# Kernel optimization log

Measured on AMD Instinct MI355X. Metric: run time of the kernel, lower is better.

## Reference

```python
import jax, jax.numpy as jnp
import numpy as np

D_MODEL = 1024
D_MEMORY = 64
CAPACITY = 65536
THETA = 0.01
MAX_GRAD_NORM = 1.0
GATE_HIDDEN = 32


def _gate(x, w1, b1, w2, b2):
    # 2-layer MLP: Linear -> SiLU -> Linear -> Sigmoid, squeeze last dim
    h = jax.nn.silu(x @ w1 + b1)
    return jax.nn.sigmoid(h @ w2 + b2)[..., 0]


def _assoc_loss(memory, k, v):
    # l(M; x) = mean((softmax(k M^T / sqrt(d)) M - v)^2)
    scores = jnp.einsum('bsd,cd->bsc', k, memory) / jnp.sqrt(jnp.asarray(D_MEMORY, k.dtype))
    w = jax.nn.softmax(scores, axis=-1)          # [B,S,capacity]
    retrieved = jnp.einsum('bsc,cd->bsd', w, memory)
    return jnp.mean((retrieved - v) ** 2)


def setup_inputs() -> dict:
    key = jax.random.key(0)
    ks = jax.random.split(key, 16)
    x = jax.random.normal(ks[0], (2, 1024, D_MODEL), dtype=jnp.float32)
    memory = jax.random.normal(ks[1], (CAPACITY, D_MEMORY), dtype=jnp.float32) * 0.02
    momentum_S = jax.random.normal(ks[2], (CAPACITY, D_MEMORY), dtype=jnp.float32) * 0.01
    # projections (stored as [in, out]; torch Linear applies x @ W.T + b)
    Wk = jax.random.normal(ks[3], (D_MODEL, D_MEMORY), dtype=jnp.float32) * 0.02
    bk = jnp.zeros((D_MEMORY,), dtype=jnp.float32)
    Wv = jax.random.normal(ks[4], (D_MODEL, D_MEMORY), dtype=jnp.float32) * 0.02
    bv = jnp.zeros((D_MEMORY,), dtype=jnp.float32)
    # forget gate MLP
    fg_w1 = jax.random.normal(ks[5], (D_MODEL, GATE_HIDDEN), dtype=jnp.float32) * 0.02
    fg_b1 = jnp.zeros((GATE_HIDDEN,), dtype=jnp.float32)
    fg_w2 = jax.random.normal(ks[6], (GATE_HIDDEN, 1), dtype=jnp.float32) * 0.02
    fg_b2 = jnp.zeros((1,), dtype=jnp.float32)
    # decay gate MLP
    dg_w1 = jax.random.normal(ks[7], (D_MODEL, GATE_HIDDEN), dtype=jnp.float32) * 0.02
    dg_b1 = jnp.zeros((GATE_HIDDEN,), dtype=jnp.float32)
    dg_w2 = jax.random.normal(ks[8], (GATE_HIDDEN, 1), dtype=jnp.float32) * 0.02
    dg_b2 = jnp.zeros((1,), dtype=jnp.float32)
    return {
        'x': x, 'memory': memory, 'momentum_S': momentum_S,
        'Wk': Wk, 'bk': bk, 'Wv': Wv, 'bv': bv,
        'fg_w1': fg_w1, 'fg_b1': fg_b1, 'fg_w2': fg_w2, 'fg_b2': fg_b2,
        'dg_w1': dg_w1, 'dg_b1': dg_b1, 'dg_w2': dg_w2, 'dg_b2': dg_b2,
    }


def reference(x, memory, momentum_S, Wk, bk, Wv, bv,
              fg_w1, fg_b1, fg_w2, fg_b2, dg_w1, dg_b1, dg_w2, dg_b2):
    # NeuralMemory.update(x): surprise-gradient momentum write with gated decay
    k = x @ Wk + bk   # [B,S,d_memory]
    v = x @ Wv + bv
    loss, grad_M = jax.value_and_grad(lambda M: _assoc_loss(M, k, v))(memory)
    # gradient clipping to max norm 1.0
    gn = jnp.linalg.norm(grad_M)
    grad_M = grad_M * jnp.minimum(1.0, MAX_GRAD_NORM / gn)
    # data-dependent gates on sequence-pooled input
    x_pooled = x.mean(axis=1)                                # [B, d_model]
    alpha_t = _gate(x_pooled, fg_w1, fg_b1, fg_w2, fg_b2).mean()
    eta_t = _gate(x_pooled, dg_w1, dg_b1, dg_w2, dg_b2).mean()
    # S_t = eta * S_{t-1} - theta * grad; M_t = (1 - alpha) * M_{t-1} + S_t
    S_new = eta_t * momentum_S - THETA * grad_M
    M_new = (1.0 - alpha_t) * memory + S_new
    return loss, M_new, S_new
```

## Files before the change

### kernel.cpp

```cpp
#include <hip/hip_runtime.h>
#include <math.h>

#define D_MODEL 1024
#define DMEM 64
#define CAP 65536
#define SEQ 1024
#define NTOT 2048
#define GATE_H 32
#define THETA 0.01f
#define ISQD 0.125f
#define LOG2E 1.4426950408889634f
#define LN2 0.6931471805599453f
#define NSPLIT 8
#define CSPL (CAP / NSPLIT)
#define GN_BLOCKS 2048

typedef float f32x4 __attribute__((ext_vector_type(4)));
typedef short bf16x8 __attribute__((ext_vector_type(8)));
typedef unsigned int u32x4 __attribute__((ext_vector_type(4)));
typedef unsigned int u32x2 __attribute__((ext_vector_type(2)));

#define MFMA16(a, b, c) __builtin_amdgcn_mfma_f32_16x16x32_bf16(a, b, c, 0, 0, 0)

__device__ inline unsigned short f2bf(float f) {
  union { float f; unsigned u; } v; v.f = f;
  unsigned r = v.u + 0x7FFFu + ((v.u >> 16) & 1u);
  return (unsigned short)(r >> 16);
}
__device__ inline unsigned cvtpk(float lo, float hi) {
  unsigned r;
  asm("v_cvt_pk_bf16_f32 %0, %1, %2" : "=v"(r) : "v"(lo), "v"(hi));
  return r;
}
__device__ inline float exp2i(float x) {
  float r;
  asm("v_exp_f32 %0, %1" : "=v"(r) : "v"(x));
  return r;
}

__global__ __launch_bounds__(256) void k_packm(const float* __restrict__ mem,
                                               unsigned short* __restrict__ Msb,
                                               unsigned short* __restrict__ MsbT) {
  __shared__ __align__(16) short tile[64][72];
  int tid = threadIdx.x;
  int c0 = blockIdx.x * 64;
  int r = tid >> 2, dp = (tid & 3) * 16;
  const float4* src = (const float4*)(mem + (size_t)(c0 + r) * DMEM + dp);
  float4 q0 = src[0], q1 = src[1], q2 = src[2], q3 = src[3];
  float va[16] = {q0.x, q0.y, q0.z, q0.w, q1.x, q1.y, q1.z, q1.w,
                  q2.x, q2.y, q2.z, q2.w, q3.x, q3.y, q3.z, q3.w};
  const float s1 = ISQD * LOG2E;
  union { unsigned short s[16]; u32x4 v[2]; } o;
#pragma unroll
  for (int j = 0; j < 16; ++j) o.s[j] = f2bf(va[j] * s1);
  *(u32x4*)(Msb + (size_t)(c0 + r) * DMEM + dp) = o.v[0];
  *(u32x4*)(Msb + (size_t)(c0 + r) * DMEM + dp + 8) = o.v[1];
#pragma unroll
  for (int j = 0; j < 16; ++j) tile[dp + j][r] = (short)f2bf(va[j] * ISQD);
  __syncthreads();
  int d2 = tid >> 2, cp = (tid & 3) * 16;
  u32x4 t0 = *(const u32x4*)&tile[d2][cp];
  u32x4 t1 = *(const u32x4*)&tile[d2][cp + 8];
  *(u32x4*)(MsbT + (size_t)d2 * CAP + c0 + cp) = t0;
  *(u32x4*)(MsbT + (size_t)d2 * CAP + c0 + cp + 8) = t1;
}

__global__ __launch_bounds__(256) void k_proj(const float* __restrict__ x,
    const float* __restrict__ Wk, const float* __restrict__ bk,
    const float* __restrict__ Wv, const float* __restrict__ bv,
    float* __restrict__ vout,
    unsigned short* __restrict__ kb, unsigned short* __restrict__ kbT) {
  __shared__ __align__(16) float xs[4 * D_MODEL];
  int tid = threadIdx.x;
  int r = tid >> 6, j = tid & 63;
  int nb = blockIdx.x * 4;
  const float4* xr = (const float4*)(x + (size_t)nb * D_MODEL);
  float4* xs4 = (float4*)xs;
#pragma unroll
  for (int q = 0; q < 4; ++q) xs4[tid + 256 * q] = xr[tid + 256 * q];
  __syncthreads();
  float ak = bk[j], av = bv[j];
  const float* xrow = xs + r * D_MODEL;
#pragma unroll 8
  for (int i = 0; i < D_MODEL; ++i) {
    float xv = xrow[i];
    ak = fmaf(xv, Wk[i * DMEM + j], ak);
    av = fmaf(xv, Wv[i * DMEM + j], av);
  }
  int n = nb + r;
  vout[n * DMEM + j] = av;
  kb[n * DMEM + j] = f2bf(ak);
  kbT[(size_t)j * NTOT + n] = f2bf(ak * LN2);
}

__global__ __launch_bounds__(256) void k_pool(const float* __restrict__ x,
                                              float* __restrict__ pooled) {
  int idx = blockIdx.x * 256 + threadIdx.x;
  int b = idx >> 10, j = idx & 1023;
  const float* base = x + (size_t)b * SEQ * D_MODEL + j;
  float s = 0.f;
  for (int t = 0; t < SEQ; ++t) s += base[(size_t)t * D_MODEL];
  pooled[idx] = s * (1.0f / SEQ);
}

__global__ __launch_bounds__(128) void k_gates(const float* __restrict__ pooled,
    const float* __restrict__ fw1, const float* __restrict__ fb1,
    const float* __restrict__ fw2, const float* __restrict__ fb2,
    const float* __restrict__ dw1, const float* __restrict__ db1,
    const float* __restrict__ dw2, const float* __restrict__ db2,
    float* __restrict__ scal) {
  __shared__ float hsh[2][2][GATE_H];
  __shared__ float outs[2][2];
  int t = threadIdx.x;
  int gate = t >> 6, b = (t >> 5) & 1, h = t & 31;
  const float* w1 = gate ? dw1 : fw1;
  const float* b1 = gate ? db1 : fb1;
  float z = b1[h];
  const float* prow = pooled + b * D_MODEL;
  for (int i = 0; i < D_MODEL; ++i) z = fmaf(prow[i], w1[i * GATE_H + h], z);
  float sig = 1.f / (1.f + __expf(-z));
  hsh[gate][b][h] = z * sig;
  __syncthreads();
  if (t < 4) {
    int gg = t >> 1, bb = t & 1;
    const float* w2 = gg ? dw2 : fw2;
    float zz = gg ? db2[0] : fb2[0];
    for (int hh = 0; hh < GATE_H; ++hh) zz += hsh[gg][bb][hh] * w2[hh];
    outs[gg][bb] = 1.f / (1.f + __expf(-zz));
  }
  __syncthreads();
  if (t == 0) {
    scal[0] = 0.5f * (outs[0][0] + outs[0][1]);
    scal[1] = 0.5f * (outs[1][0] + outs[1][1]);
  }
}

__global__ __launch_bounds__(256, 2) void k_fwd4(
    const unsigned short* __restrict__ kb,
    const unsigned short* __restrict__ Msb,
    const unsigned short* __restrict__ MsbT,
    float* __restrict__ l_s, float* __restrict__ r_s) {
  __shared__ __align__(16) char smem[46080];
  short* Mt  = (short*)smem;
  short* MTt = Mt + 128 * 72;
  unsigned* wtb = (unsigned*)(MTt + 64 * 136);
  int tid = threadIdx.x;
  int wv = tid >> 6, lane = tid & 63;
  int u = lane >> 4, p = lane & 15;
  int sp = blockIdx.x & 7, ng = blockIdx.x >> 3;
  int n0 = ng * 32;
  unsigned* wtp = wtb + wv * 640;

  bf16x8 bkf[2][2];
#pragma unroll
  for (int nf = 0; nf < 2; ++nf) {
    const unsigned short* kbase = kb + (size_t)(n0 + nf * 16 + p) * DMEM + u * 8;
    bkf[nf][0] = *(const bf16x8*)(kbase);
    bkf[nf][1] = *(const bf16x8*)(kbase + 32);
  }

  int mc = tid >> 3, mdh = tid & 7;
  int td = tid >> 4, tch = tid & 15;
  int c0base = sp * CSPL;
  u32x4 sM[4], sT[4];
#pragma unroll
  for (int q = 0; q < 4; ++q) {
    sM[q] = *(const u32x4*)(Msb + (size_t)(c0base + mc + 32 * q) * DMEM + mdh * 8);
    sT[q] = *(const u32x4*)(MsbT + (size_t)(td + 16 * q) * CAP + c0base + tch * 8);
  }

  f32x4 racc[4][2];
#pragma unroll
  for (int df = 0; df < 4; ++df)
#pragma unroll
    for (int nf = 0; nf < 2; ++nf) racc[df][nf] = (f32x4){0.f, 0.f, 0.f, 0.f};
  float esum0 = 0.f, esum1 = 0.f;

  const int NT = CSPL / 128;
  for (int it = 0; it < NT; ++it) {
    __syncthreads();
#pragma unroll
    for (int q = 0; q < 4; ++q) {
      *(u32x4*)(Mt + (mc + 32 * q) * 72 + mdh * 8) = sM[q];
      *(u32x4*)(MTt + (td + 16 * q) * 136 + tch * 8) = sT[q];
    }
    __syncthreads();
    int itn = (it + 1 < NT) ? it + 1 : it;
    int c0n = c0base + itn * 128;
#pragma unroll
    for (int q = 0; q < 4; ++q) {
      sM[q] = *(const u32x4*)(Msb + (size_t)(c0n + mc + 32 * q) * DMEM + mdh * 8);
      sT[q] = *(const u32x4*)(MsbT + (size_t)(td + 16 * q) * CAP + c0n + tch * 8);
    }
    f32x4 s[2][2];
#pragma unroll
    for (int cf = 0; cf < 2; ++cf) {
      bf16x8 a0 = *(const bf16x8*)(Mt + (wv * 32 + cf * 16 + p) * 72 + u * 8);
      bf16x8 a1 = *(const bf16x8*)(Mt + (wv * 32 + cf * 16 + p) * 72 + 32 + u * 8);
#pragma unroll
      for (int nf = 0; nf < 2; ++nf) {
        f32x4 acc = (f32x4){0.f, 0.f, 0.f, 0.f};
        acc = MFMA16(a0, bkf[nf][0], acc);
        acc = MFMA16(a1, bkf[nf][1], acc);
        s[cf][nf] = acc;
      }
    }
    asm volatile("" ::: "memory");
#pragma unroll
    for (int cf = 0; cf < 2; ++cf)
#pragma unroll
      for (int nf = 0; nf < 2; ++nf) {
        float e0 = exp2i(s[cf][nf].x), e1 = exp2i(s[cf][nf].y);
        float e2 = exp2i(s[cf][nf].z), e3 = exp2i(s[cf][nf].w);
        if (nf == 0) esum0 += (e0 + e1) + (e2 + e3);
        else         esum1 += (e0 + e1) + (e2 + e3);
        wtp[(nf * 16 + p) * 20 + cf * 8 + 2 * u]     = cvtpk(e0, e1);
        wtp[(nf * 16 + p) * 20 + cf * 8 + 2 * u + 1] = cvtpk(e2, e3);
      }
    asm volatile("" ::: "memory");
    u32x4 bw0 = *(const u32x4*)(wtp + p * 20 + u * 4);
    u32x4 bw1 = *(const u32x4*)(wtp + (16 + p) * 20 + u * 4);
    asm volatile("" ::: "memory");
    bf16x8 w0 = __builtin_bit_cast(bf16x8, bw0);
    bf16x8 w1 = __builtin_bit_cast(bf16x8, bw1);
#pragma unroll
    for (int df = 0; df < 4; ++df) {
      bf16x8 aT = *(const bf16x8*)(MTt + (df * 16 + p) * 136 + wv * 32 + u * 8);
      racc[df][0] = MFMA16(aT, w0, racc[df][0]);
      racc[df][1] = MFMA16(aT, w1, racc[df][1]);
    }
  }

  esum0 += __shfl_xor(esum0, 16, 64);
  esum0 += __shfl_xor(esum0, 32, 64);
  esum1 += __shfl_xor(esum1, 16, 64);
  esum1 += __shfl_xor(esum1, 32, 64);
  if (u == 0) {
    l_s[(sp * 4 + wv) * NTOT + n0 + p] = esum0;
    l_s[(sp * 4 + wv) * NTOT + n0 + 16 + p] = esum1;
  }

  __syncthreads();
  float* rt = (float*)smem;
#pragma unroll
  for (int df = 0; df < 4; ++df)
#pragma unroll
    for (int nf = 0; nf < 2; ++nf)
#pragma unroll
      for (int r = 0; r < 4; ++r)
        rt[(wv * 64 + df * 16 + 4 * u + r) * 33 + nf * 16 + p] = racc[df][nf][r];
  __syncthreads();
  int n = tid >> 3;
  int d8 = (tid & 7) * 8;
  float o[8];
#pragma unroll
  for (int q = 0; q < 8; ++q)
    o[q] = (rt[(0 * 64 + d8 + q) * 33 + n] + rt[(1 * 64 + d8 + q) * 33 + n]) +
           (rt[(2 * 64 + d8 + q) * 33 + n] + rt[(3 * 64 + d8 + q) * 33 + n]);
  float* dst = r_s + ((size_t)sp * NTOT + n0 + n) * DMEM + d8;
  *(float4*)(dst) = (float4){o[0], o[1], o[2], o[3]};
  *(float4*)(dst + 4) = (float4){o[4], o[5], o[6], o[7]};
}

__global__ __launch_bounds__(256) void k_comb(
    const float* __restrict__ l_s, const float* __restrict__ r_s,
    const float* __restrict__ v,
    unsigned short* __restrict__ gb, unsigned short* __restrict__ gbT,
    float* __restrict__ gdr8, float* __restrict__ linv,
    float* __restrict__ lossp) {
  __shared__ float lsum[4];
  int tid = threadIdx.x;
  int nl = tid >> 6, dd = tid & 63;
  int n = blockIdx.x * 4 + nl;
  float l = 0.f;
#pragma unroll
  for (int s = 0; s < 32; ++s) l += l_s[s * NTOT + n];
  float r = 0.f;
#pragma unroll
  for (int s = 0; s < NSPLIT; ++s)
    r += r_s[((size_t)s * NTOT + n) * DMEM + dd];
  float li = 1.f / l;
  float ret = r * li * 8.0f;
  float vv = v[n * DMEM + dd];
  const float c0 = 2.f / (float)(NTOT * DMEM);
  float diff = ret - vv;
  float gv = c0 * diff;
  gb[n * DMEM + dd] = f2bf(gv);
  gbT[dd * NTOT + n] = f2bf(gv);
  float gr = gv * ret;
  float lp = diff * diff;
#pragma unroll
  for (int off = 1; off < 64; off <<= 1) {
    gr += __shfl_xor(gr, off, 64);
    lp += __shfl_xor(lp, off, 64);
  }
  if (dd == 0) {
    gdr8[n] = gr * (ISQD * LOG2E);
    linv[n] = li;
    lsum[nl] = lp;
  }
  __syncthreads();
  if (tid == 0)
    lossp[blockIdx.x] =
        (lsum[0] + lsum[1] + lsum[2] + lsum[3]) * (1.f / (float)(NTOT * DMEM));
}

__global__ __launch_bounds__(256, 2) void k_bwd7(
    const unsigned short* __restrict__ kb, const unsigned short* __restrict__ kbT,
    const unsigned short* __restrict__ gb, const unsigned short* __restrict__ gbT,
    const unsigned short* __restrict__ Msb,
    const float* __restrict__ linv, const float* __restrict__ gdr8,
    float* __restrict__ gradf, unsigned short* __restrict__ gradh) {
  __shared__ __align__(16) short kt[32][72];
  __shared__ __align__(16) short gt[32][72];
  __shared__ __align__(16) short tT[2][64][40];
  __shared__ unsigned wct[4][2][1280];
  int tid = threadIdx.x;
  int wv = tid >> 6, lane = tid & 63;
  int u = lane >> 4, p = lane & 15;
  int half = blockIdx.x & 1;
  int cw = (blockIdx.x >> 1) * 256 + wv * 64;
  int nbase = half * (NTOT / 2);
  unsigned* wtp = wct[wv][0];
  unsigned* ctp = wct[wv][1];

  bf16x8 bM[4][2];
#pragma unroll
  for (int cf = 0; cf < 4; ++cf) {
    const unsigned short* mb = Msb + (size_t)(cw + cf * 16 + p) * DMEM + u * 8;
    bM[cf][0] = *(const bf16x8*)(mb);
    bM[cf][1] = *(const bf16x8*)(mb + 32);
  }

  f32x4 gacc[4][4];
#pragma unroll
  for (int cf = 0; cf < 4; ++cf)
#pragma unroll
    for (int df = 0; df < 4; ++df) gacc[cf][df] = (f32x4){0.f, 0.f, 0.f, 0.f};

  int sn = tid >> 3, sdh = tid & 7;
  int sd = tid >> 2, sch = tid & 3;

  u32x4 rk  = *(const u32x4*)(kb + (size_t)(nbase + sn) * DMEM + sdh * 8);
  u32x4 rg  = *(const u32x4*)(gb + (size_t)(nbase + sn) * DMEM + sdh * 8);
  u32x4 rkT = *(const u32x4*)(kbT + (size_t)sd * NTOT + nbase + sch * 8);
  u32x4 rgT = *(const u32x4*)(gbT + (size_t)sd * NTOT + nbase + sch * 8);

  const int NT = (NTOT / 2) / 32;
  for (int it = 0; it < NT; ++it) {
    int n0 = nbase + it * 32;
    __syncthreads();
    *(u32x4*)&kt[sn][sdh * 8] = rk;
    *(u32x4*)&gt[sn][sdh * 8] = rg;
    *(u32x4*)&tT[0][sd][sch * 8] = rkT;
    *(u32x4*)&tT[1][sd][sch * 8] = rgT;
    __syncthreads();
    {
      int n0n = (it + 1 < NT) ? n0 + 32 : n0;
      rk  = *(const u32x4*)(kb + (size_t)(n0n + sn) * DMEM + sdh * 8);
      rg  = *(const u32x4*)(gb + (size_t)(n0n + sn) * DMEM + sdh * 8);
      rkT = *(const u32x4*)(kbT + (size_t)sd * NTOT + n0n + sch * 8);
      rgT = *(const u32x4*)(gbT + (size_t)sd * NTOT + n0n + sch * 8);
    }
    asm volatile("" ::: "memory");
#pragma unroll
    for (int nf = 0; nf < 2; ++nf) {
      bf16x8 ka0 = *(const bf16x8*)&kt[nf * 16 + p][u * 8];
      bf16x8 ka1 = *(const bf16x8*)&kt[nf * 16 + p][u * 8 + 32];
      bf16x8 ga0 = *(const bf16x8*)&gt[nf * 16 + p][u * 8];
      bf16x8 ga1 = *(const bf16x8*)&gt[nf * 16 + p][u * 8 + 32];
      float4 lv = *(const float4*)(linv + n0 + nf * 16 + u * 4);
      float4 dv = *(const float4*)(gdr8 + n0 + nf * 16 + u * 4);
#pragma unroll
      for (int cf = 0; cf < 4; ++cf) {
        f32x4 s = (f32x4){0.f, 0.f, 0.f, 0.f};
        s = MFMA16(ka0, bM[cf][0], s);
        s = MFMA16(ka1, bM[cf][1], s);
        f32x4 pg = (f32x4){0.f, 0.f, 0.f, 0.f};
        pg = MFMA16(ga0, bM[cf][0], pg);
        pg = MFMA16(ga1, bM[cf][1], pg);
        float w0 = exp2i(s.x) * lv.x;
        float w1 = exp2i(s.y) * lv.y;
        float w2 = exp2i(s.z) * lv.z;
        float w3 = exp2i(s.w) * lv.w;
        float c0v = w0 * (pg.x - dv.x);
        float c1v = w1 * (pg.y - dv.y);
        float c2v = w2 * (pg.z - dv.z);
        float c3v = w3 * (pg.w - dv.w);
        wtp[(cf * 16 + p) * 20 + nf * 8 + 2 * u]     = cvtpk(w0, w1);
        wtp[(cf * 16 + p) * 20 + nf * 8 + 2 * u + 1] = cvtpk(w2, w3);
        ctp[(cf * 16 + p) * 20 + nf * 8 + 2 * u]     = cvtpk(c0v, c1v);
        ctp[(cf * 16 + p) * 20 + nf * 8 + 2 * u + 1] = cvtpk(c2v, c3v);
      }
    }
    asm volatile("" ::: "memory");
    u32x4 aw4[4], ac4[4];
#pragma unroll
    for (int cf = 0; cf < 4; ++cf) {
      aw4[cf] = *(const u32x4*)(wtp + (cf * 16 + p) * 20 + u * 4);
      ac4[cf] = *(const u32x4*)(ctp + (cf * 16 + p) * 20 + u * 4);
    }
    asm volatile("" ::: "memory");
#pragma unroll
    for (int df = 0; df < 4; ++df) {
      bf16x8 bg = *(const bf16x8*)&tT[1][df * 16 + p][u * 8];
      bf16x8 bk2 = *(const bf16x8*)&tT[0][df * 16 + p][u * 8];
#pragma unroll
      for (int cf = 0; cf < 4; ++cf) {
        gacc[cf][df] = MFMA16(__builtin_bit_cast(bf16x8, aw4[cf]), bg, gacc[cf][df]);
        gacc[cf][df] = MFMA16(__builtin_bit_cast(bf16x8, ac4[cf]), bk2, gacc[cf][df]);
      }
    }
  }

  if (half == 0) {
#pragma unroll
    for (int cf = 0; cf < 4; ++cf)
#pragma unroll
      for (int df = 0; df < 4; ++df)
#pragma unroll
        for (int r = 0; r < 4; ++r)
          gradf[(size_t)(cw + cf * 16 + 4 * u + r) * DMEM + df * 16 + p] =
              gacc[cf][df][r];
  } else {
#pragma unroll
    for (int cf = 0; cf < 4; ++cf)
#pragma unroll
      for (int df = 0; df < 4; ++df)
#pragma unroll
        for (int r = 0; r < 4; ++r)
          gradh[(size_t)(cw + cf * 16 + 4 * u + r) * DMEM + df * 16 + p] =
              f2bf(gacc[cf][df][r]);
  }
}

__global__ __launch_bounds__(256) void k_gcomb(float* __restrict__ grad,
                                               const unsigned short* __restrict__ gradh,
                                               float* __restrict__ gnsqp) {
  __shared__ float red[4];
  int tid = threadIdx.x;
  size_t base = (size_t)blockIdx.x * 2048 + tid;
  float ss = 0.f;
#pragma unroll
  for (int j = 0; j < 8; ++j) {
    size_t i = base + (size_t)j * 256;
    unsigned hv = ((unsigned)gradh[i]) << 16;
    float v = grad[i] + __builtin_bit_cast(float, hv);
    grad[i] = v;
    ss = fmaf(v, v, ss);
  }
#pragma unroll
  for (int off = 1; off < 64; off <<= 1) ss += __shfl_xor(ss, off, 64);
  if ((tid & 63) == 0) red[tid >> 6] = ss;
  __syncthreads();
  if (tid == 0) gnsqp[blockIdx.x] = (red[0] + red[1]) + (red[2] + red[3]);
}

__global__ __launch_bounds__(256) void k_fin(const float* __restrict__ gnsqp,
                                             const float* __restrict__ lossp,
                                             float* __restrict__ scal) {
  __shared__ float sh[8];
  int tid = threadIdx.x;
  float s1 = 0.f, s2 = 0.f;
  for (int i = tid; i < GN_BLOCKS; i += 256) s1 += gnsqp[i];
  for (int i = tid; i < NTOT / 4; i += 256) s2 += lossp[i];
#pragma unroll
  for (int off = 1; off < 64; off <<= 1) {
    s1 += __shfl_xor(s1, off, 64);
    s2 += __shfl_xor(s2, off, 64);
  }
  if ((tid & 63) == 0) { sh[(tid >> 6) * 2] = s1; sh[(tid >> 6) * 2 + 1] = s2; }
  __syncthreads();
  if (tid == 0) {
    float gnsq = sh[0] + sh[2] + sh[4] + sh[6];
    float loss = sh[1] + sh[3] + sh[5] + sh[7];
    float gn = sqrtf(gnsq);
    float clip = (gn > 1.0f) ? (1.0f / gn) : 1.0f;
    scal[2] = THETA * clip;
    scal[3] = loss;
  }
}

__global__ __launch_bounds__(256) void k_upd(const float* __restrict__ mem,
    const float* __restrict__ momS, const float* __restrict__ grad,
    const float* __restrict__ scal, float* __restrict__ dout) {
  size_t i = (size_t)blockIdx.x * 256 + threadIdx.x;
  float oma = 1.f - scal[0];
  float eta = scal[1];
  float th = scal[2];
  if (i == 0) dout[0] = scal[3];
  float gr = grad[i];
  float sn = fmaf(-th, gr, eta * momS[i]);
  dout[1 + (size_t)CAP * DMEM + i] = sn;
  dout[1 + i] = fmaf(oma, mem[i], sn);
}

extern "C" void kernel_launch(void* const* d_in, const int* in_sizes, int n_in,
                              void* d_out, int out_size, void* d_ws, size_t ws_size,
                              hipStream_t stream) {
  const float* x    = (const float*)d_in[0];
  const float* mem  = (const float*)d_in[1];
  const float* momS = (const float*)d_in[2];
  const float* Wk   = (const float*)d_in[3];
  const float* bk   = (const float*)d_in[4];
  const float* Wv   = (const float*)d_in[5];
  const float* bv   = (const float*)d_in[6];
  const float* fw1  = (const float*)d_in[7];
  const float* fb1  = (const float*)d_in[8];
  const float* fw2  = (const float*)d_in[9];
  const float* fb2  = (const float*)d_in[10];
  const float* dw1  = (const float*)d_in[11];
  const float* db1  = (const float*)d_in[12];
  const float* dw2  = (const float*)d_in[13];
  const float* db2  = (const float*)d_in[14];

  float* out = (float*)d_out;
  float* wsf = (float*)d_ws;

  float* scal   = wsf;
  float* pooled = wsf + 16;
  float* vbuf   = wsf + 2064;
  float* gdr8   = vbuf + 131072;
  float* linvb  = gdr8 + 2048;
  float* lsb    = linvb + 2048;
  float* lossp  = lsb + 65536;
  float* gnsqp  = lossp + 512;
  unsigned short* kb  = (unsigned short*)(gnsqp + 2048);
  unsigned short* kbT = kb + 131072;
  unsigned short* gb  = kbT + 131072;
  unsigned short* gbT = gb + 131072;

  unsigned short* Msb   = (unsigned short*)out;
  unsigned short* MsbT  = Msb + (size_t)CAP * DMEM;
  unsigned short* gradh = MsbT;
  float* rsb  = out + 4 + (size_t)CAP * DMEM + 4;
  float* grad = out + 1 + (size_t)CAP * DMEM;

  k_packm<<<CAP / 64, 256, 0, stream>>>(mem, Msb, MsbT);
  k_proj <<<NTOT / 4, 256, 0, stream>>>(x, Wk, bk, Wv, bv, vbuf, kb, kbT);
  k_pool <<<8, 256, 0, stream>>>(x, pooled);
  k_gates<<<1, 128, 0, stream>>>(pooled, fw1, fb1, fw2, fb2, dw1, db1, dw2, db2, scal);
  k_fwd4 <<<(NTOT / 32) * NSPLIT, 256, 0, stream>>>(kb, Msb, MsbT, lsb, rsb);
  k_comb <<<NTOT / 4, 256, 0, stream>>>(lsb, rsb, vbuf, gb, gbT, gdr8, linvb, lossp);
  k_bwd7 <<<(CAP / 256) * 2, 256, 0, stream>>>(kb, kbT, gb, gbT, Msb, linvb, gdr8, grad, gradh);
  k_gcomb<<<GN_BLOCKS, 256, 0, stream>>>(grad, gradh, gnsqp);
  k_fin  <<<1, 256, 0, stream>>>(gnsqp, lossp, scal);
  k_upd  <<<(CAP * DMEM) / 256, 256, 0, stream>>>(mem, momS, grad, scal, out);
}
```

Baseline: 303.4 us.

## Raise occupancy of forward and backward kernels by shrinking per-wave tiles

The forward kernel now builds the softmax weight tile one n-fragment at a time, so the per-wave LDS staging buffer is halved and the MT fragments are hoisted into registers. Launch bounds move from 2 to 4 blocks per CU. The backward kernel halves its capacity tile per wave (64 to 32 rows), doubling the grid and halving accumulator registers and LDS so that 4 blocks per CU fit. The aim is more waves resident to hide latency, at the cost of more blocks re-reading the k/g streams in backward and extra LDS round trips in forward.

```diff
diff --git a/kernel.cpp b/kernel.cpp
--- a/kernel.cpp
+++ b/kernel.cpp
@@ -135,12 +135,12 @@
   }
 }
 
-__global__ __launch_bounds__(256, 2) void k_fwd4(
+__global__ __launch_bounds__(256, 4) void k_fwd8(
     const unsigned short* __restrict__ kb,
     const unsigned short* __restrict__ Msb,
     const unsigned short* __restrict__ MsbT,
     float* __restrict__ l_s, float* __restrict__ r_s) {
-  __shared__ __align__(16) char smem[46080];
+  __shared__ __align__(16) char smem[40960];
   short* Mt  = (short*)smem;
   short* MTt = Mt + 128 * 72;
   unsigned* wtb = (unsigned*)(MTt + 64 * 136);
@@ -149,7 +149,7 @@
   int u = lane >> 4, p = lane & 15;
   int sp = blockIdx.x & 7, ng = blockIdx.x >> 3;
   int n0 = ng * 32;
-  unsigned* wtp = wtb + wv * 640;
+  unsigned* wtp = wtb + wv * 320;
 
   bf16x8 bkf[2][2];
 #pragma unroll
@@ -205,29 +205,29 @@
         s[cf][nf] = acc;
       }
     }
+    bf16x8 aTf[4];
+#pragma unroll
+    for (int df = 0; df < 4; ++df)
+      aTf[df] = *(const bf16x8*)(MTt + (df * 16 + p) * 136 + wv * 32 + u * 8);
     asm volatile("" ::: "memory");
 #pragma unroll
-    for (int cf = 0; cf < 2; ++cf)
-#pragma unroll
-      for (int nf = 0; nf < 2; ++nf) {
+    for (int nf = 0; nf < 2; ++nf) {
+#pragma unroll
+      for (int cf = 0; cf < 2; ++cf) {
         float e0 = exp2i(s[cf][nf].x), e1 = exp2i(s[cf][nf].y);
         float e2 = exp2i(s[cf][nf].z), e3 = exp2i(s[cf][nf].w);
         if (nf == 0) esum0 += (e0 + e1) + (e2 + e3);
         else         esum1 += (e0 + e1) + (e2 + e3);
-        wtp[(nf * 16 + p) * 20 + cf * 8 + 2 * u]     = cvtpk(e0, e1);
-        wtp[(nf * 16 + p) * 20 + cf * 8 + 2 * u + 1] = cvtpk(e2, e3);
+        wtp[p * 20 + cf * 8 + 2 * u]     = cvtpk(e0, e1);
+        wtp[p * 20 + cf * 8 + 2 * u + 1] = cvtpk(e2, e3);
       }
-    asm volatile("" ::: "memory");
-    u32x4 bw0 = *(const u32x4*)(wtp + p * 20 + u * 4);
-    u32x4 bw1 = *(const u32x4*)(wtp + (16 + p) * 20 + u * 4);
-    asm volatile("" ::: "memory");
-    bf16x8 w0 = __builtin_bit_cast(bf16x8, bw0);
-    bf16x8 w1 = __builtin_bit_cast(bf16x8, bw1);
-#pragma unroll
-    for (int df = 0; df < 4; ++df) {
-      bf16x8 aT = *(const bf16x8*)(MTt + (df * 16 + p) * 136 + wv * 32 + u * 8);
-      racc[df][0] = MFMA16(aT, w0, racc[df][0]);
-      racc[df][1] = MFMA16(aT, w1, racc[df][1]);
+      asm volatile("" ::: "memory");
+      u32x4 bw = *(const u32x4*)(wtp + p * 20 + u * 4);
+      asm volatile("" ::: "memory");
+      bf16x8 w = __builtin_bit_cast(bf16x8, bw);
+#pragma unroll
+      for (int df = 0; df < 4; ++df)
+        racc[df][nf] = MFMA16(aTf[df], w, racc[df][nf]);
     }
   }
 
@@ -305,7 +305,7 @@
         (lsum[0] + lsum[1] + lsum[2] + lsum[3]) * (1.f / (float)(NTOT * DMEM));
 }
 
-__global__ __launch_bounds__(256, 2) void k_bwd7(
+__global__ __launch_bounds__(256, 4) void k_bwd8(
     const unsigned short* __restrict__ kb, const unsigned short* __restrict__ kbT,
     const unsigned short* __restrict__ gb, const unsigned short* __restrict__ gbT,
     const unsigned short* __restrict__ Msb,
@@ -314,27 +314,27 @@
   __shared__ __align__(16) short kt[32][72];
   __shared__ __align__(16) short gt[32][72];
   __shared__ __align__(16) short tT[2][64][40];
-  __shared__ unsigned wct[4][2][1280];
+  __shared__ unsigned wct[4][2][640];
   int tid = threadIdx.x;
   int wv = tid >> 6, lane = tid & 63;
   int u = lane >> 4, p = lane & 15;
   int half = blockIdx.x & 1;
-  int cw = (blockIdx.x >> 1) * 256 + wv * 64;
+  int cw = (blockIdx.x >> 1) * 128 + wv * 32;
   int nbase = half * (NTOT / 2);
   unsigned* wtp = wct[wv][0];
   unsigned* ctp = wct[wv][1];
 
-  bf16x8 bM[4][2];
-#pragma unroll
-  for (int cf = 0; cf < 4; ++cf) {
+  bf16x8 bM[2][2];
+#pragma unroll
+  for (int cf = 0; cf < 2; ++cf) {
     const unsigned short* mb = Msb + (size_t)(cw + cf * 16 + p) * DMEM + u * 8;
     bM[cf][0] = *(const bf16x8*)(mb);
     bM[cf][1] = *(const bf16x8*)(mb + 32);
   }
 
-  f32x4 gacc[4][4];
-#pragma unroll
-  for (int cf = 0; cf < 4; ++cf)
+  f32x4 gacc[2][4];
+#pragma unroll
+  for (int cf = 0; cf < 2; ++cf)
 #pragma unroll
     for (int df = 0; df < 4; ++df) gacc[cf][df] = (f32x4){0.f, 0.f, 0.f, 0.f};
 
@@ -372,7 +372,7 @@
       float4 lv = *(const float4*)(linv + n0 + nf * 16 + u * 4);
       float4 dv = *(const float4*)(gdr8 + n0 + nf * 16 + u * 4);
 #pragma unroll
-      for (int cf = 0; cf < 4; ++cf) {
+      for (int cf = 0; cf < 2; ++cf) {
         f32x4 s = (f32x4){0.f, 0.f, 0.f, 0.f};
         s = MFMA16(ka0, bM[cf][0], s);
         s = MFMA16(ka1, bM[cf][1], s);
@@ -394,9 +394,9 @@
       }
     }
     asm volatile("" ::: "memory");
-    u32x4 aw4[4], ac4[4];
-#pragma unroll
-    for (int cf = 0; cf < 4; ++cf) {
+    u32x4 aw4[2], ac4[2];
+#pragma unroll
+    for (int cf = 0; cf < 2; ++cf) {
       aw4[cf] = *(const u32x4*)(wtp + (cf * 16 + p) * 20 + u * 4);
       ac4[cf] = *(const u32x4*)(ctp + (cf * 16 + p) * 20 + u * 4);
     }
@@ -406,7 +406,7 @@
       bf16x8 bg = *(const bf16x8*)&tT[1][df * 16 + p][u * 8];
       bf16x8 bk2 = *(const bf16x8*)&tT[0][df * 16 + p][u * 8];
 #pragma unroll
-      for (int cf = 0; cf < 4; ++cf) {
+      for (int cf = 0; cf < 2; ++cf) {
         gacc[cf][df] = MFMA16(__builtin_bit_cast(bf16x8, aw4[cf]), bg, gacc[cf][df]);
         gacc[cf][df] = MFMA16(__builtin_bit_cast(bf16x8, ac4[cf]), bk2, gacc[cf][df]);
       }
@@ -415,7 +415,7 @@
 
   if (half == 0) {
 #pragma unroll
-    for (int cf = 0; cf < 4; ++cf)
+    for (int cf = 0; cf < 2; ++cf)
 #pragma unroll
       for (int df = 0; df < 4; ++df)
 #pragma unroll
@@ -424,7 +424,7 @@
               gacc[cf][df][r];
   } else {
 #pragma unroll
-    for (int cf = 0; cf < 4; ++cf)
+    for (int cf = 0; cf < 2; ++cf)
 #pragma unroll
       for (int df = 0; df < 4; ++df)
 #pragma unroll
@@ -540,9 +540,9 @@
   k_proj <<<NTOT / 4, 256, 0, stream>>>(x, Wk, bk, Wv, bv, vbuf, kb, kbT);
   k_pool <<<8, 256, 0, stream>>>(x, pooled);
   k_gates<<<1, 128, 0, stream>>>(pooled, fw1, fb1, fw2, fb2, dw1, db1, dw2, db2, scal);
-  k_fwd4 <<<(NTOT / 32) * NSPLIT, 256, 0, stream>>>(kb, Msb, MsbT, lsb, rsb);
+  k_fwd8 <<<(NTOT / 32) * NSPLIT, 256, 0, stream>>>(kb, Msb, MsbT, lsb, rsb);
   k_comb <<<NTOT / 4, 256, 0, stream>>>(lsb, rsb, vbuf, gb, gbT, gdr8, linvb, lossp);
-  k_bwd7 <<<(CAP / 256) * 2, 256, 0, stream>>>(kb, kbT, gb, gbT, Msb, linvb, gdr8, grad, gradh);
+  k_bwd8 <<<(CAP / 128) * 2, 256, 0, stream>>>(kb, kbT, gb, gbT, Msb, linvb, gdr8, grad, gradh);
   k_gcomb<<<GN_BLOCKS, 256, 0, stream>>>(grad, gradh, gnsqp);
   k_fin  <<<1, 256, 0, stream>>>(gnsqp, lossp, scal);
   k_upd  <<<(CAP * DMEM) / 256, 256, 0, stream>>>(mem, momS, grad, scal, out);
```

New measurement: 366.3 us. 1.21x slower.

## Double forward split count, raise occupancy, shrink softmax-weight scratch and reduce l in-block

Applied to the files above, without the earlier changes.

The forward attention kernel now splits capacity into 16 chunks instead of 8, launching twice as many blocks. It targets 4 blocks per CU by halving the per-wave weight staging buffer: exp weights are staged one query fragment at a time, and the MT fragments are preloaded into registers. Row sums are reduced across waves in shared memory before being written, so the combine kernel reads 16 partials per row instead of 32. The trade-off is more r_s partial traffic for the combine kernel and tighter register pressure under the higher occupancy bound.

```diff
diff --git a/kernel.cpp b/kernel.cpp
--- a/kernel.cpp
+++ b/kernel.cpp
@@ -11,7 +11,7 @@
 #define ISQD 0.125f
 #define LOG2E 1.4426950408889634f
 #define LN2 0.6931471805599453f
-#define NSPLIT 8
+#define NSPLIT 16
 #define CSPL (CAP / NSPLIT)
 #define GN_BLOCKS 2048
 
@@ -135,21 +135,21 @@
   }
 }
 
-__global__ __launch_bounds__(256, 2) void k_fwd4(
+__global__ __launch_bounds__(256, 4) void k_fwd9(
     const unsigned short* __restrict__ kb,
     const unsigned short* __restrict__ Msb,
     const unsigned short* __restrict__ MsbT,
     float* __restrict__ l_s, float* __restrict__ r_s) {
-  __shared__ __align__(16) char smem[46080];
+  __shared__ __align__(16) char smem[40960];
   short* Mt  = (short*)smem;
   short* MTt = Mt + 128 * 72;
   unsigned* wtb = (unsigned*)(MTt + 64 * 136);
   int tid = threadIdx.x;
   int wv = tid >> 6, lane = tid & 63;
   int u = lane >> 4, p = lane & 15;
-  int sp = blockIdx.x & 7, ng = blockIdx.x >> 3;
+  int sp = blockIdx.x & 15, ng = blockIdx.x >> 4;
   int n0 = ng * 32;
-  unsigned* wtp = wtb + wv * 640;
+  unsigned* wtp = wtb + wv * 320;
 
   bf16x8 bkf[2][2];
 #pragma unroll
@@ -205,42 +205,48 @@
         s[cf][nf] = acc;
       }
     }
+    bf16x8 aTf[4];
+#pragma unroll
+    for (int df = 0; df < 4; ++df)
+      aTf[df] = *(const bf16x8*)(MTt + (df * 16 + p) * 136 + wv * 32 + u * 8);
     asm volatile("" ::: "memory");
 #pragma unroll
-    for (int cf = 0; cf < 2; ++cf)
-#pragma unroll
-      for (int nf = 0; nf < 2; ++nf) {
+    for (int nf = 0; nf < 2; ++nf) {
+#pragma unroll
+      for (int cf = 0; cf < 2; ++cf) {
         float e0 = exp2i(s[cf][nf].x), e1 = exp2i(s[cf][nf].y);
         float e2 = exp2i(s[cf][nf].z), e3 = exp2i(s[cf][nf].w);
         if (nf == 0) esum0 += (e0 + e1) + (e2 + e3);
         else         esum1 += (e0 + e1) + (e2 + e3);
-        wtp[(nf * 16 + p) * 20 + cf * 8 + 2 * u]     = cvtpk(e0, e1);
-        wtp[(nf * 16 + p) * 20 + cf * 8 + 2 * u + 1] = cvtpk(e2, e3);
+        wtp[p * 20 + cf * 8 + 2 * u]     = cvtpk(e0, e1);
+        wtp[p * 20 + cf * 8 + 2 * u + 1] = cvtpk(e2, e3);
       }
-    asm volatile("" ::: "memory");
-    u32x4 bw0 = *(const u32x4*)(wtp + p * 20 + u * 4);
-    u32x4 bw1 = *(const u32x4*)(wtp + (16 + p) * 20 + u * 4);
-    asm volatile("" ::: "memory");
-    bf16x8 w0 = __builtin_bit_cast(bf16x8, bw0);
-    bf16x8 w1 = __builtin_bit_cast(bf16x8, bw1);
-#pragma unroll
-    for (int df = 0; df < 4; ++df) {
-      bf16x8 aT = *(const bf16x8*)(MTt + (df * 16 + p) * 136 + wv * 32 + u * 8);
-      racc[df][0] = MFMA16(aT, w0, racc[df][0]);
-      racc[df][1] = MFMA16(aT, w1, racc[df][1]);
-    }
-  }
-
+      asm volatile("" ::: "memory");
+      u32x4 bw = *(const u32x4*)(wtp + p * 20 + u * 4);
+      asm volatile("" ::: "memory");
+      bf16x8 w = __builtin_bit_cast(bf16x8, bw);
+#pragma unroll
+      for (int df = 0; df < 4; ++df)
+        racc[df][nf] = MFMA16(aTf[df], w, racc[df][nf]);
+    }
+  }
+
+  __syncthreads();
   esum0 += __shfl_xor(esum0, 16, 64);
   esum0 += __shfl_xor(esum0, 32, 64);
   esum1 += __shfl_xor(esum1, 16, 64);
   esum1 += __shfl_xor(esum1, 32, 64);
+  float* esh = (float*)wtb;
   if (u == 0) {
-    l_s[(sp * 4 + wv) * NTOT + n0 + p] = esum0;
-    l_s[(sp * 4 + wv) * NTOT + n0 + 16 + p] = esum1;
-  }
-
-  __syncthreads();
+    esh[wv * 32 + p] = esum0;
+    esh[wv * 32 + 16 + p] = esum1;
+  }
+  __syncthreads();
+  if (tid < 32) {
+    float l = (esh[0 * 32 + tid] + esh[1 * 32 + tid]) +
+              (esh[2 * 32 + tid] + esh[3 * 32 + tid]);
+    l_s[sp * NTOT + n0 + tid] = l;
+  }
   float* rt = (float*)smem;
 #pragma unroll
   for (int df = 0; df < 4; ++df)
@@ -274,7 +280,7 @@
   int n = blockIdx.x * 4 + nl;
   float l = 0.f;
 #pragma unroll
-  for (int s = 0; s < 32; ++s) l += l_s[s * NTOT + n];
+  for (int s = 0; s < NSPLIT; ++s) l += l_s[s * NTOT + n];
   float r = 0.f;
 #pragma unroll
   for (int s = 0; s < NSPLIT; ++s)
@@ -523,7 +529,7 @@
   float* gdr8   = vbuf + 131072;
   float* linvb  = gdr8 + 2048;
   float* lsb    = linvb + 2048;
-  float* lossp  = lsb + 65536;
+  float* lossp  = lsb + 32768;
   float* gnsqp  = lossp + 512;
   unsigned short* kb  = (unsigned short*)(gnsqp + 2048);
   unsigned short* kbT = kb + 131072;
@@ -540,7 +546,7 @@
   k_proj <<<NTOT / 4, 256, 0, stream>>>(x, Wk, bk, Wv, bv, vbuf, kb, kbT);
   k_pool <<<8, 256, 0, stream>>>(x, pooled);
   k_gates<<<1, 128, 0, stream>>>(pooled, fw1, fb1, fw2, fb2, dw1, db1, dw2, db2, scal);
-  k_fwd4 <<<(NTOT / 32) * NSPLIT, 256, 0, stream>>>(kb, Msb, MsbT, lsb, rsb);
+  k_fwd9 <<<(NTOT / 32) * NSPLIT, 256, 0, stream>>>(kb, Msb, MsbT, lsb, rsb);
   k_comb <<<NTOT / 4, 256, 0, stream>>>(lsb, rsb, vbuf, gb, gbT, gdr8, linvb, lossp);
   k_bwd7 <<<(CAP / 256) * 2, 256, 0, stream>>>(kb, kbT, gb, gbT, Msb, linvb, gdr8, grad, gradh);
   k_gcomb<<<GN_BLOCKS, 256, 0, stream>>>(grad, gradh, gnsqp);
```

Result: slower. 332.1 us (+9.5%).
